# Performance work log

Measured on AMD Instinct MI355X. Metric: run time of the kernel, lower is better.

## Reference

```python
import jax, jax.numpy as jnp
import numpy as np

N_NODES = 50000
IN_CH = 512
OUT_CH = 128
N_EDGES = 1_600_000


def setup_inputs() -> dict:
    key = jax.random.key(0)
    k1, k2, k3, k4 = jax.random.split(key, 4)
    x = jax.random.normal(k1, (N_NODES, IN_CH), dtype=jnp.float32)
    edge_index = jax.random.randint(k2, (2, N_EDGES), 0, N_NODES, dtype=jnp.int64)
    # GCNConv params (weight [in, out], bias [out]); decoder Linear(out, in, bias=False) -> weight [in, out] used as z @ W_dec
    W_enc = jax.random.normal(k3, (IN_CH, OUT_CH), dtype=jnp.float32) * 0.05
    b_enc = jnp.zeros((OUT_CH,), dtype=jnp.float32)
    W_dec = jax.random.normal(k4, (OUT_CH, IN_CH), dtype=jnp.float32) * 0.05
    return {"x": x, "edge_index": edge_index, "W_enc": W_enc, "b_enc": b_enc, "W_dec": W_dec}


def reference(x, edge_index, W_enc, b_enc, W_dec):
    N = x.shape[0]
    # --- GCNConv: add self-loops, symmetric normalization, gather-scale-scatter ---
    loops = jnp.arange(N, dtype=edge_index.dtype)
    src = jnp.concatenate([edge_index[0], loops])  # message sources
    dst = jnp.concatenate([edge_index[1], loops])  # aggregation targets
    deg = jax.ops.segment_sum(jnp.ones_like(dst, dtype=x.dtype), dst, num_segments=N)
    deg_inv_sqrt = jnp.where(deg > 0, jax.lax.rsqrt(jnp.maximum(deg, 1.0)), 0.0)
    norm = deg_inv_sqrt[src] * deg_inv_sqrt[dst]  # [E+N]
    xw = x @ W_enc                                 # [N, OUT]
    msg = xw[src] * norm[:, None]                  # gather + scale
    z = jax.ops.segment_sum(msg, dst, num_segments=N) + b_enc  # scatter-add
    # --- decode head: relu -> linear (no bias) -> softmax over features ---
    z = jax.nn.relu(z)
    logits = z @ W_dec                             # [N, IN]
    return jax.nn.softmax(logits, axis=1)
```

## Files before the change

### kernel.cpp

```cpp
#include <hip/hip_runtime.h>
#include <stdint.h>

#define NN   50000
#define INC  512
#define OUTC 128
#define NB   782
#define CAP  4096
#define NWG  256

typedef unsigned int  uint;
typedef unsigned short u16;
typedef short bf16x8 __attribute__((ext_vector_type(8)));
typedef float f32x4  __attribute__((ext_vector_type(4)));
typedef u16   u16x8  __attribute__((ext_vector_type(8)));
typedef u16   u16x4  __attribute__((ext_vector_type(4)));

__device__ __forceinline__ u16 f2bf(float f) {
  uint u = __float_as_uint(f);
  u += 0x7fffu + ((u >> 16) & 1u);
  return (u16)(u >> 16);
}
__device__ __forceinline__ float bflo(uint v) { return __uint_as_float(v << 16); }
__device__ __forceinline__ float bfhi(uint v) { return __uint_as_float(v & 0xffff0000u); }

__global__ __launch_bounds__(256) void k_scatter_pairs(const int* __restrict__ src,
                                                       const int* __restrict__ dst, int E,
                                                       uint* __restrict__ bucket_cursor,
                                                       uint* __restrict__ pairs) {
  __shared__ uint hist[NB];
  __shared__ uint base[NB];
  __shared__ uint cur[NB];
  const int t = threadIdx.x;
  const int chunk = (E + NWG - 1) / NWG;
  const int e0 = blockIdx.x * chunk;
  const int e1 = min(e0 + chunk, E);

  for (int i = t; i < NB; i += 256) hist[i] = 0;
  __syncthreads();
  for (int e = e0 + t; e < e1; e += 256) {
    int b = dst[e] >> 6;
    atomicAdd(&hist[b], 1u);
  }
  __syncthreads();
  for (int i = t; i < NB; i += 256) {
    uint c = hist[i];
    base[i] = c ? atomicAdd(&bucket_cursor[i * 16], c) : 0u;
    cur[i] = 0;
  }
  __syncthreads();
  for (int e = e0 + t; e < e1; e += 256) {
    int d = dst[e];
    int b = d >> 6;
    uint r = atomicAdd(&cur[b], 1u);
    uint off = base[b] + r;
    if (off < CAP) pairs[(size_t)b * CAP + off] = (uint)src[e] | ((uint)(d & 63) << 6 << 10);
  }
}

__global__ __launch_bounds__(256) void k_sort(const uint* __restrict__ bucket_cursor,
                                              const uint* __restrict__ pairs,
                                              uint* __restrict__ csr,
                                              uint* __restrict__ rs_packed,
                                              float* __restrict__ dis) {
  __shared__ uint plist[CAP];
  __shared__ uint slist[CAP];
  __shared__ uint cnt[64], pfx[64], cur[64];
  const int b = blockIdx.x, t = threadIdx.x;
  uint n_e = bucket_cursor[b * 16]; if (n_e > CAP) n_e = CAP;

  if (t < 64) cnt[t] = 0;
  __syncthreads();
  for (uint e = t; e < n_e; e += 256) {
    uint v = pairs[(size_t)b * CAP + e];
    plist[e] = v;
    atomicAdd(&cnt[(v >> 16) & 63u], 1u);
  }
  __syncthreads();
  if (t == 0) {
    uint run = 0;
    for (int i = 0; i < 64; ++i) { pfx[i] = run; run += cnt[i]; }
  }
  __syncthreads();
  if (t < 64) {
    cur[t] = pfx[t];
    int n = b * 64 + t;
    if (n < NN) {
      rs_packed[n] = pfx[t] | (cnt[t] << 16);
      dis[n] = rsqrtf((float)cnt[t] + 1.0f);
    }
  }
  __syncthreads();
  for (uint e = t; e < n_e; e += 256) {
    uint v = plist[e];
    uint pos = atomicAdd(&cur[(v >> 16) & 63u], 1u);
    slist[pos] = v & 0xffffu;
  }
  __syncthreads();
  for (uint e = t; e < n_e; e += 256) csr[(size_t)b * CAP + e] = slist[e];
}

__global__ __launch_bounds__(256) void k_prep_enc(const float* __restrict__ W,
                                                  uint8_t* __restrict__ outw) {
  __shared__ float t[32][128];
  const int tid = threadIdx.x;
  const int k0 = blockIdx.x * 32;
#pragma unroll
  for (int r = 0; r < 16; ++r) {
    int e = r * 256 + tid;
    int kk = e >> 7, n = e & 127;
    t[kk][n] = W[(size_t)(k0 + kk) * 128 + n];
  }
  __syncthreads();
#pragma unroll
  for (int it = 0; it < 2; ++it) {
    int item = it * 256 + tid;
    int n = item & 127, kc = item >> 7;
    int kg = k0 + kc * 8;
    int q = kg >> 7, kin = kg & 127;
    u16x8 p;
#pragma unroll
    for (int j = 0; j < 8; ++j) p[j] = f2bf(t[kc * 8 + j][n]);
    *(u16x8*)(outw + q * 32768 + ((((uint)n * 256) + (uint)kin * 2) ^ (uint)((n & 7) << 4))) = p;
  }
}
__global__ __launch_bounds__(256) void k_prep_dec(const float* __restrict__ W,
                                                  uint8_t* __restrict__ outw) {
  __shared__ float t[128][32];
  const int tid = threadIdx.x;
  const int n0 = blockIdx.x * 32;
#pragma unroll
  for (int r = 0; r < 16; ++r) {
    int e = r * 256 + tid;
    int k = e >> 5, nl = e & 31;
    t[k][nl] = W[(size_t)k * 512 + n0 + nl];
  }
  __syncthreads();
#pragma unroll
  for (int it = 0; it < 2; ++it) {
    int item = it * 256 + tid;
    int nl = item & 31, kc = item >> 5;
    int n = n0 + nl;
    int c = n >> 7, nin = n & 127;
    u16x8 p;
#pragma unroll
    for (int j = 0; j < 8; ++j) p[j] = f2bf(t[kc * 8 + j][nl]);
    *(u16x8*)(outw + c * 32768 + ((((uint)nin * 256) + (uint)kc * 16) ^ (uint)((nin & 7) << 4))) = p;
  }
}

__global__ __launch_bounds__(256, 2) void k_gemm1(const float* __restrict__ x,
                                                  const uint8_t* __restrict__ WtE,
                                                  const float* __restrict__ dis,
                                                  u16* __restrict__ xws) {
  __shared__ __align__(16) uint8_t lds[49152];
  uint8_t* WL = lds;
  uint8_t* XL = lds + 32768;
  const int tid = threadIdx.x, lane = tid & 63, wv = tid >> 6;
  const int lane15 = lane & 15, laneh = lane >> 4;
  const int rb = blockIdx.x * 128;

  f32x4 acc[2][8];
#pragma unroll
  for (int m = 0; m < 2; ++m)
#pragma unroll
    for (int n = 0; n < 8; ++n) acc[m][n] = (f32x4){0.f, 0.f, 0.f, 0.f};

  const int srow = tid >> 1;
  int grow = rb + srow; if (grow >= NN) grow = NN - 1;
  const int khalf = (tid & 1) * 32;
  const uint xb  = (uint)srow * 128 + (uint)khalf * 2;
  const uint xsw = (uint)((srow & 7) << 4);
  const int ar0 = wv * 32 + lane15, ar1 = ar0 + 16;

  for (int q = 0; q < 4; ++q) {
    __syncthreads();
    { const u16x8* s = (const u16x8*)(WtE + q * 32768);
      u16x8* d = (u16x8*)WL;
#pragma unroll
      for (int i = 0; i < 8; ++i) d[tid + i * 256] = s[tid + i * 256]; }
#pragma unroll
    for (int step = 0; step < 2; ++step) {
      if (step) __syncthreads();
      const float4* xs = (const float4*)(x + (size_t)grow * INC + q * 128 + step * 64 + khalf);
      float4 v[8];
#pragma unroll
      for (int j = 0; j < 8; ++j) v[j] = xs[j];
#pragma unroll
      for (int j = 0; j < 8; ++j) {
        u16x4 p; p.x = f2bf(v[j].x); p.y = f2bf(v[j].y); p.z = f2bf(v[j].z); p.w = f2bf(v[j].w);
        *(u16x4*)(XL + ((xb + j * 8) ^ xsw)) = p;
      }
      __syncthreads();
#pragma unroll
      for (int kk = 0; kk < 2; ++kk) {
        bf16x8 a0 = *(const bf16x8*)(XL + (((uint)ar0 * 128 + kk * 64 + laneh * 16) ^ (uint)((ar0 & 7) << 4)));
        bf16x8 a1 = *(const bf16x8*)(XL + (((uint)ar1 * 128 + kk * 64 + laneh * 16) ^ (uint)((ar1 & 7) << 4)));
#pragma unroll
        for (int nf = 0; nf < 8; ++nf) {
          int n = nf * 16 + lane15;
          bf16x8 b = *(const bf16x8*)(WL + (((uint)n * 256 + step * 128 + kk * 64 + laneh * 16) ^ (uint)((n & 7) << 4)));
          acc[0][nf] = __builtin_amdgcn_mfma_f32_16x16x32_bf16(a0, b, acc[0][nf], 0, 0, 0);
          acc[1][nf] = __builtin_amdgcn_mfma_f32_16x16x32_bf16(a1, b, acc[1][nf], 0, 0, 0);
        }
      }
    }
  }
#pragma unroll
  for (int m = 0; m < 2; ++m) {
#pragma unroll
    for (int r = 0; r < 4; ++r) {
      int row = rb + wv * 32 + m * 16 + laneh * 4 + r;
      if (row < NN) {
        float dv = dis[row];
#pragma unroll
        for (int nf = 0; nf < 8; ++nf)
          xws[(size_t)row * 128 + nf * 16 + lane15] = f2bf(acc[m][nf][r] * dv);
      }
    }
  }
}

__global__ __launch_bounds__(64) void k_aggregate(const u16* __restrict__ xws,
                                                  const float* __restrict__ dis,
                                                  const uint* __restrict__ rs_packed,
                                                  const uint* __restrict__ csr,
                                                  const float* __restrict__ bias,
                                                  uint8_t* __restrict__ zsw) {
  const int i = blockIdx.x, lane = threadIdx.x;
  const uint v = rs_packed[i];
  const uint s0 = (uint)(i >> 6) * CAP + (v & 0xffffu);
  const uint s1 = s0 + (v >> 16);

  float a0 = 0.f, a1 = 0.f;
  uint j = s0;
  for (; j + 3 < s1; j += 4) {
    uint i0 = csr[j], i1 = csr[j + 1], i2 = csr[j + 2], i3 = csr[j + 3];
    uint v0 = *(const uint*)(xws + (size_t)i0 * 128 + lane * 2);
    uint v1 = *(const uint*)(xws + (size_t)i1 * 128 + lane * 2);
    uint v2 = *(const uint*)(xws + (size_t)i2 * 128 + lane * 2);
    uint v3 = *(const uint*)(xws + (size_t)i3 * 128 + lane * 2);
    a0 += bflo(v0) + bflo(v1) + bflo(v2) + bflo(v3);
    a1 += bfhi(v0) + bfhi(v1) + bfhi(v2) + bfhi(v3);
  }
  for (; j < s1; ++j) {
    uint vv = *(const uint*)(xws + (size_t)csr[j] * 128 + lane * 2);
    a0 += bflo(vv); a1 += bfhi(vv);
  }
  uint vs = *(const uint*)(xws + (size_t)i * 128 + lane * 2);
  float di = dis[i];
  float2 bb = *(const float2*)(bias + lane * 2);
  float z0 = fmaxf(di * (a0 + bflo(vs)) + bb.x, 0.f);
  float z1 = fmaxf(di * (a1 + bfhi(vs)) + bb.y, 0.f);
  uint pk = (uint)f2bf(z0) | ((uint)f2bf(z1) << 16);
  *(uint*)(zsw + ((((uint)i * 256) + (uint)lane * 4) ^ (uint)((i & 7) << 4))) = pk;
}

__global__ __launch_bounds__(512, 2) void k_decode(const uint8_t* __restrict__ zsw,
                                                   const uint8_t* __restrict__ WtD,
                                                   float* __restrict__ out) {
  __shared__ __align__(16) uint8_t lds[65536];
  uint8_t* ZL = lds;
  uint8_t* WL = lds + 32768;
  const int tid = threadIdx.x, lane = tid & 63, wv = tid >> 6;
  const int lane15 = lane & 15, laneh = lane >> 4;
  const int rb = blockIdx.x * 128;

  { const u16x8* s = (const u16x8*)(zsw + (size_t)rb * 256);
    u16x8* d = (u16x8*)ZL;
#pragma unroll
    for (int i = 0; i < 4; ++i) d[tid + i * 512] = s[tid + i * 512]; }

  f32x4 acc[32];
#pragma unroll
  for (int f = 0; f < 32; ++f) acc[f] = (f32x4){0.f, 0.f, 0.f, 0.f};

  const int zr = wv * 16 + lane15;
  bf16x8 a[4];

#pragma unroll
  for (int c = 0; c < 4; ++c) {
    if (c) __syncthreads();
    { const u16x8* s = (const u16x8*)(WtD + c * 32768);
      u16x8* d = (u16x8*)WL;
#pragma unroll
      for (int i = 0; i < 4; ++i) d[tid + i * 512] = s[tid + i * 512]; }
    __syncthreads();
    if (c == 0) {
#pragma unroll
      for (int s = 0; s < 4; ++s)
        a[s] = *(const bf16x8*)(ZL + (((uint)zr * 256 + s * 64 + laneh * 16) ^ (uint)((zr & 7) << 4)));
    }
#pragma unroll
    for (int nf = 0; nf < 8; ++nf) {
      int n = nf * 16 + lane15;
      uint nb = (uint)n * 256 + laneh * 16, nsw = (uint)((n & 7) << 4);
#pragma unroll
      for (int s = 0; s < 4; ++s) {
        bf16x8 bfr = *(const bf16x8*)(WL + ((nb + s * 64) ^ nsw));
        acc[c * 8 + nf] = __builtin_amdgcn_mfma_f32_16x16x32_bf16(a[s], bfr, acc[c * 8 + nf], 0, 0, 0);
      }
    }
  }

#pragma unroll
  for (int r = 0; r < 4; ++r) {
    float m = acc[0][r];
#pragma unroll
    for (int f = 1; f < 32; ++f) m = fmaxf(m, acc[f][r]);
    m = fmaxf(m, __shfl_xor(m, 1)); m = fmaxf(m, __shfl_xor(m, 2));
    m = fmaxf(m, __shfl_xor(m, 4)); m = fmaxf(m, __shfl_xor(m, 8));
    float sum = 0.f;
#pragma unroll
    for (int f = 0; f < 32; ++f) { acc[f][r] = __expf(acc[f][r] - m); sum += acc[f][r]; }
    sum += __shfl_xor(sum, 1); sum += __shfl_xor(sum, 2);
    sum += __shfl_xor(sum, 4); sum += __shfl_xor(sum, 8);
    float inv = 1.0f / sum;
    int row = rb + wv * 16 + laneh * 4 + r;
    if (row < NN) {
      float* op = out + (size_t)row * INC + lane15;
#pragma unroll
      for (int f = 0; f < 32; ++f)
        op[(f >> 3) * 128 + (f & 7) * 16] = acc[f][r] * inv;
    }
  }
}

extern "C" void kernel_launch(void* const* d_in, const int* in_sizes, int n_in,
                              void* d_out, int out_size, void* d_ws, size_t ws_size,
                              hipStream_t stream) {
  const float* x     = (const float*)d_in[0];
  const int*   ei    = (const int*)d_in[1];
  const float* W_enc = (const float*)d_in[2];
  const float* b_enc = (const float*)d_in[3];
  const float* W_dec = (const float*)d_in[4];
  float* out = (float*)d_out;

  const int E = in_sizes[1] / 2;
  const int* esrc = ei;
  const int* edst = ei + E;

  uint8_t* ws = (uint8_t*)d_ws;
  uint*  bucket_cursor = (uint*)(ws);
  uint*  pairs         = (uint*)(ws + 0x10000);
  uint*  csr           = (uint*)(ws + 0xC80000);
  uint*  rs_packed     = (uint*)(ws + 0x1900000);
  float* dis           = (float*)(ws + 0x1940000);
  uint8_t* WtE         = ws + 0x1980000;
  uint8_t* WtD         = ws + 0x19A0000;
  u16*   xws           = (u16*)(ws + 0x19C0000);
  uint8_t* zsw         = ws + 0x2600000;

  hipMemsetAsync(bucket_cursor, 0, NB * 64, stream);
  k_scatter_pairs<<<NWG, 256, 0, stream>>>(esrc, edst, E, bucket_cursor, pairs);
  k_sort         <<<NB, 256, 0, stream>>>(bucket_cursor, pairs, csr, rs_packed, dis);
  k_prep_enc     <<<16, 256, 0, stream>>>(W_enc, WtE);
  k_prep_dec     <<<16, 256, 0, stream>>>(W_dec, WtD);
  k_gemm1        <<<(NN + 127) / 128, 256, 0, stream>>>(x, WtE, dis, xws);
  k_aggregate    <<<NN, 64, 0, stream>>>(xws, dis, rs_packed, csr, b_enc, zsw);
  k_decode       <<<(NN + 127) / 128, 512, 0, stream>>>(zsw, WtD, out);
}
```

Before: 339.8 us.

## Use direct global-to-LDS loads, merge weight prep, retile decode and aggregate

```diff
diff --git a/kernel.cpp b/kernel.cpp
--- a/kernel.cpp
+++ b/kernel.cpp
@@ -22,6 +22,12 @@
 }
 __device__ __forceinline__ float bflo(uint v) { return __uint_as_float(v << 16); }
 __device__ __forceinline__ float bfhi(uint v) { return __uint_as_float(v & 0xffff0000u); }
+
+__device__ __forceinline__ void gl_lds16(const void* g, void* l) {
+  __builtin_amdgcn_global_load_lds(
+      (const __attribute__((address_space(1))) uint*)g,
+      (__attribute__((address_space(3))) uint*)l, 16, 0, 0);
+}
 
 __global__ __launch_bounds__(256) void k_scatter_pairs(const int* __restrict__ src,
                                                        const int* __restrict__ dst, int E,
@@ -53,7 +59,7 @@
     int b = d >> 6;
     uint r = atomicAdd(&cur[b], 1u);
     uint off = base[b] + r;
-    if (off < CAP) pairs[(size_t)b * CAP + off] = (uint)src[e] | ((uint)(d & 63) << 6 << 10);
+    if (off < CAP) pairs[(size_t)b * CAP + off] = (uint)src[e] | ((uint)(d & 63) << 16);
   }
 }
 
@@ -99,52 +105,52 @@
   for (uint e = t; e < n_e; e += 256) csr[(size_t)b * CAP + e] = slist[e];
 }
 
-__global__ __launch_bounds__(256) void k_prep_enc(const float* __restrict__ W,
-                                                  uint8_t* __restrict__ outw) {
-  __shared__ float t[32][128];
+__global__ __launch_bounds__(256) void k_prep(const float* __restrict__ We,
+                                              const float* __restrict__ Wd,
+                                              uint8_t* __restrict__ oE,
+                                              uint8_t* __restrict__ oD) {
+  __shared__ float t[4096];
   const int tid = threadIdx.x;
-  const int k0 = blockIdx.x * 32;
-#pragma unroll
-  for (int r = 0; r < 16; ++r) {
-    int e = r * 256 + tid;
-    int kk = e >> 7, n = e & 127;
-    t[kk][n] = W[(size_t)(k0 + kk) * 128 + n];
-  }
-  __syncthreads();
-#pragma unroll
-  for (int it = 0; it < 2; ++it) {
-    int item = it * 256 + tid;
-    int n = item & 127, kc = item >> 7;
-    int kg = k0 + kc * 8;
-    int q = kg >> 7, kin = kg & 127;
-    u16x8 p;
-#pragma unroll
-    for (int j = 0; j < 8; ++j) p[j] = f2bf(t[kc * 8 + j][n]);
-    *(u16x8*)(outw + q * 32768 + ((((uint)n * 256) + (uint)kin * 2) ^ (uint)((n & 7) << 4))) = p;
-  }
-}
-__global__ __launch_bounds__(256) void k_prep_dec(const float* __restrict__ W,
-                                                  uint8_t* __restrict__ outw) {
-  __shared__ float t[128][32];
-  const int tid = threadIdx.x;
-  const int n0 = blockIdx.x * 32;
-#pragma unroll
-  for (int r = 0; r < 16; ++r) {
-    int e = r * 256 + tid;
-    int k = e >> 5, nl = e & 31;
-    t[k][nl] = W[(size_t)k * 512 + n0 + nl];
-  }
-  __syncthreads();
-#pragma unroll
-  for (int it = 0; it < 2; ++it) {
-    int item = it * 256 + tid;
-    int nl = item & 31, kc = item >> 5;
-    int n = n0 + nl;
-    int c = n >> 7, nin = n & 127;
-    u16x8 p;
-#pragma unroll
-    for (int j = 0; j < 8; ++j) p[j] = f2bf(t[kc * 8 + j][nl]);
-    *(u16x8*)(outw + c * 32768 + ((((uint)nin * 256) + (uint)kc * 16) ^ (uint)((nin & 7) << 4))) = p;
+  if (blockIdx.x < 16) {
+    const int k0 = blockIdx.x * 32;
+#pragma unroll
+    for (int r = 0; r < 16; ++r) {
+      int e = r * 256 + tid;
+      int kk = e >> 7, n = e & 127;
+      t[kk * 128 + n] = We[(size_t)(k0 + kk) * 128 + n];
+    }
+    __syncthreads();
+#pragma unroll
+    for (int it = 0; it < 2; ++it) {
+      int item = it * 256 + tid;
+      int n = item & 127, kc = item >> 7;
+      int kg = k0 + kc * 8;
+      int q = kg >> 7, kin = kg & 127;
+      u16x8 p;
+#pragma unroll
+      for (int j = 0; j < 8; ++j) p[j] = f2bf(t[(kc * 8 + j) * 128 + n]);
+      *(u16x8*)(oE + q * 32768 + ((((uint)n * 256) + (uint)kin * 2) ^ (uint)((n & 7) << 4))) = p;
+    }
+  } else {
+    const int n0 = (blockIdx.x - 16) * 32;
+#pragma unroll
+    for (int r = 0; r < 16; ++r) {
+      int e = r * 256 + tid;
+      int k = e >> 5, nl = e & 31;
+      t[k * 32 + nl] = Wd[(size_t)k * 512 + n0 + nl];
+    }
+    __syncthreads();
+#pragma unroll
+    for (int it = 0; it < 2; ++it) {
+      int item = it * 256 + tid;
+      int nl = item & 31, kc = item >> 5;
+      int n = n0 + nl;
+      int c = n >> 7, nin = n & 127;
+      u16x8 p;
+#pragma unroll
+      for (int j = 0; j < 8; ++j) p[j] = f2bf(t[(kc * 8 + j) * 32 + nl]);
+      *(u16x8*)(oD + c * 32768 + ((((uint)nin * 256) + (uint)kc * 16) ^ (uint)((nin & 7) << 4))) = p;
+    }
   }
 }
 
@@ -174,10 +180,10 @@
 
   for (int q = 0; q < 4; ++q) {
     __syncthreads();
-    { const u16x8* s = (const u16x8*)(WtE + q * 32768);
-      u16x8* d = (u16x8*)WL;
-#pragma unroll
-      for (int i = 0; i < 8; ++i) d[tid + i * 256] = s[tid + i * 256]; }
+    { const uint8_t* s = WtE + q * 32768;
+#pragma unroll
+      for (int i = 0; i < 8; ++i)
+        gl_lds16(s + tid * 16 + i * 4096, WL + tid * 16 + i * 4096); }
 #pragma unroll
     for (int step = 0; step < 2; ++step) {
       if (step) __syncthreads();
@@ -220,27 +226,28 @@
   }
 }
 
-__global__ __launch_bounds__(64) void k_aggregate(const u16* __restrict__ xws,
-                                                  const float* __restrict__ dis,
-                                                  const uint* __restrict__ rs_packed,
-                                                  const uint* __restrict__ csr,
-                                                  const float* __restrict__ bias,
-                                                  uint8_t* __restrict__ zsw) {
-  const int i = blockIdx.x, lane = threadIdx.x;
+__global__ __launch_bounds__(128) void k_aggregate(const u16* __restrict__ xws,
+                                                   const float* __restrict__ dis,
+                                                   const uint* __restrict__ rs_packed,
+                                                   const uint* __restrict__ csr,
+                                                   const float* __restrict__ bias,
+                                                   uint8_t* __restrict__ zsw) {
+  const int i = blockIdx.x * 2 + (threadIdx.x >> 6);
+  const int lane = threadIdx.x & 63;
   const uint v = rs_packed[i];
   const uint s0 = (uint)(i >> 6) * CAP + (v & 0xffffu);
   const uint s1 = s0 + (v >> 16);
 
   float a0 = 0.f, a1 = 0.f;
   uint j = s0;
-  for (; j + 3 < s1; j += 4) {
-    uint i0 = csr[j], i1 = csr[j + 1], i2 = csr[j + 2], i3 = csr[j + 3];
-    uint v0 = *(const uint*)(xws + (size_t)i0 * 128 + lane * 2);
-    uint v1 = *(const uint*)(xws + (size_t)i1 * 128 + lane * 2);
-    uint v2 = *(const uint*)(xws + (size_t)i2 * 128 + lane * 2);
-    uint v3 = *(const uint*)(xws + (size_t)i3 * 128 + lane * 2);
-    a0 += bflo(v0) + bflo(v1) + bflo(v2) + bflo(v3);
-    a1 += bfhi(v0) + bfhi(v1) + bfhi(v2) + bfhi(v3);
+  for (; j + 7 < s1; j += 8) {
+    uint idx[8], vv[8];
+#pragma unroll
+    for (int t = 0; t < 8; ++t) idx[t] = csr[j + t];
+#pragma unroll
+    for (int t = 0; t < 8; ++t) vv[t] = *(const uint*)(xws + (size_t)idx[t] * 128 + lane * 2);
+#pragma unroll
+    for (int t = 0; t < 8; ++t) { a0 += bflo(vv[t]); a1 += bfhi(vv[t]); }
   }
   for (; j < s1; ++j) {
     uint vv = *(const uint*)(xws + (size_t)csr[j] * 128 + lane * 2);
@@ -255,20 +262,20 @@
   *(uint*)(zsw + ((((uint)i * 256) + (uint)lane * 4) ^ (uint)((i & 7) << 4))) = pk;
 }
 
-__global__ __launch_bounds__(512, 2) void k_decode(const uint8_t* __restrict__ zsw,
+__global__ __launch_bounds__(256, 2) void k_decode(const uint8_t* __restrict__ zsw,
                                                    const uint8_t* __restrict__ WtD,
                                                    float* __restrict__ out) {
-  __shared__ __align__(16) uint8_t lds[65536];
+  __shared__ __align__(16) uint8_t lds[49152];
   uint8_t* ZL = lds;
-  uint8_t* WL = lds + 32768;
+  uint8_t* WL = lds + 16384;
   const int tid = threadIdx.x, lane = tid & 63, wv = tid >> 6;
   const int lane15 = lane & 15, laneh = lane >> 4;
-  const int rb = blockIdx.x * 128;
-
-  { const u16x8* s = (const u16x8*)(zsw + (size_t)rb * 256);
-    u16x8* d = (u16x8*)ZL;
-#pragma unroll
-    for (int i = 0; i < 4; ++i) d[tid + i * 512] = s[tid + i * 512]; }
+  const int rb = blockIdx.x * 64;
+
+  { const uint8_t* s = zsw + (size_t)rb * 256;
+#pragma unroll
+    for (int i = 0; i < 4; ++i)
+      gl_lds16(s + tid * 16 + i * 4096, ZL + tid * 16 + i * 4096); }
 
   f32x4 acc[32];
 #pragma unroll
@@ -280,10 +287,10 @@
 #pragma unroll
   for (int c = 0; c < 4; ++c) {
     if (c) __syncthreads();
-    { const u16x8* s = (const u16x8*)(WtD + c * 32768);
-      u16x8* d = (u16x8*)WL;
-#pragma unroll
-      for (int i = 0; i < 4; ++i) d[tid + i * 512] = s[tid + i * 512]; }
+    { const uint8_t* s = WtD + c * 32768;
+#pragma unroll
+      for (int i = 0; i < 8; ++i)
+        gl_lds16(s + tid * 16 + i * 4096, WL + tid * 16 + i * 4096); }
     __syncthreads();
     if (c == 0) {
 #pragma unroll
@@ -353,9 +360,8 @@
   hipMemsetAsync(bucket_cursor, 0, NB * 64, stream);
   k_scatter_pairs<<<NWG, 256, 0, stream>>>(esrc, edst, E, bucket_cursor, pairs);
   k_sort         <<<NB, 256, 0, stream>>>(bucket_cursor, pairs, csr, rs_packed, dis);
-  k_prep_enc     <<<16, 256, 0, stream>>>(W_enc, WtE);
-  k_prep_dec     <<<16, 256, 0, stream>>>(W_dec, WtD);
+  k_prep         <<<32, 256, 0, stream>>>(W_enc, W_dec, WtE, WtD);
   k_gemm1        <<<(NN + 127) / 128, 256, 0, stream>>>(x, WtE, dis, xws);
-  k_aggregate    <<<NN, 64, 0, stream>>>(xws, dis, rs_packed, csr, b_enc, zsw);
-  k_decode       <<<(NN + 127) / 128, 512, 0, stream>>>(zsw, WtD, out);
-}
+  k_aggregate    <<<NN / 2, 128, 0, stream>>>(xws, dis, rs_packed, csr, b_enc, zsw);
+  k_decode       <<<(NN + 63) / 64, 256, 0, stream>>>(zsw, WtD, out);
+}
```

After: 339.7 us. Within noise of the previous version (-0.0%).
